# Performance work log

Measured on AMD Instinct MI355X. Metric: run time of the kernel, lower is better.

## Reference

```python
import jax, jax.numpy as jnp
import numpy as np
from jax import lax

DN = ('NHWC', 'HWIO', 'NHWC')

def _conv(x, k, b, stride=1):
    return lax.conv_general_dilated(x, k, (stride, stride), 'SAME', dimension_numbers=DN) + b

def _tconv(x, k, b):
    return lax.conv_transpose(x, k, (2, 2), 'SAME', dimension_numbers=DN) + b


def setup_inputs() -> dict:
    key = jax.random.key(0)
    ks = jax.random.split(key, 32)
    ki = iter(ks)
    def w(shape, scale=0.05):
        return (jax.random.normal(next(ki), shape, dtype=jnp.float32) * scale)
    inp = {}
    inp['x'] = jax.random.uniform(next(ki), (8, 128, 128, 3), dtype=jnp.float32)
    # encoder
    inp['k1'],  inp['b1']  = w((11, 11, 3, 32)),   jnp.zeros((32,), jnp.float32)
    inp['k1c'], inp['b1c'] = w((3, 3, 32, 32)),    jnp.zeros((32,), jnp.float32)
    inp['k2'],  inp['b2']  = w((11, 11, 32, 64)),  jnp.zeros((64,), jnp.float32)
    inp['k2c'], inp['b2c'] = w((3, 3, 64, 64)),    jnp.zeros((64,), jnp.float32)
    inp['k3'],  inp['b3']  = w((11, 11, 64, 128)), jnp.zeros((128,), jnp.float32)
    inp['k3c'], inp['b3c'] = w((3, 3, 128, 128)),  jnp.zeros((128,), jnp.float32)
    # codebook (codebookSize=256, latent dim 128)
    inp['codebook'] = w((256, 128), 0.1)
    # decoder
    inp['tk1'],  inp['tb1']  = w((5, 5, 128, 64)), jnp.zeros((64,), jnp.float32)
    inp['tk1c'], inp['tb1c'] = w((3, 3, 64, 64)),  jnp.zeros((64,), jnp.float32)
    inp['tk2'],  inp['tb2']  = w((5, 5, 64, 32)),  jnp.zeros((32,), jnp.float32)
    inp['tk2c'], inp['tb2c'] = w((3, 3, 32, 32)),  jnp.zeros((32,), jnp.float32)
    inp['tk3'],  inp['tb3']  = w((5, 5, 32, 32)),  jnp.zeros((32,), jnp.float32)
    inp['tk3c'], inp['tb3c'] = w((3, 3, 32, 3)),   jnp.zeros((3,), jnp.float32)
    return inp


def reference(x, k1, b1, k1c, b1c, k2, b2, k2c, b2c, k3, b3, k3c, b3c,
              codebook, tk1, tb1, tk1c, tb1c, tk2, tb2, tk2c, tb2c,
              tk3, tb3, tk3c, tb3c):
    act = jax.nn.silu  # flax.nnx.swish
    # encoder
    d1 = act(_conv(x, k1, b1, 2))
    d1 = act(_conv(d1, k1c, b1c, 1))
    d2 = act(_conv(d1, k2, b2, 2))
    d2 = act(_conv(d2, k2c, b2c, 1))
    d3 = act(_conv(d2, k3, b3, 2))
    d3 = _conv(d3, k3c, b3c, 1)               # [B, H/8, W/8, 128]
    # vector quantization: squared L2 to each codebook entry
    lat = d3.reshape(-1, 1, 128)              # [N, 1, 128]
    eu_dis = jnp.sum((lat - codebook[None]) ** 2, axis=-1)   # [N, 256]
    idx = jnp.argmin(eu_dis, axis=-1)         # [N]
    quantized = jnp.take(codebook, idx, axis=0).reshape(d3.shape)
    # straight-through estimator
    replaced = lax.stop_gradient(quantized - d3) + d3
    # decoder
    d4 = act(_tconv(replaced, tk1, tb1))
    d4 = act(_conv(d4, tk1c, tb1c, 1))
    d5 = act(_tconv(d4, tk2, tb2))
    d5 = act(_conv(d5, tk2c, tb2c, 1))
    d6 = act(_tconv(d5, tk3, tb3))
    out = _conv(d6, tk3c, tb3c, 1)            # [B, H, W, 3]
    return out
```

## Files before the change

### kernel.cpp

```cpp
#include <hip/hip_runtime.h>

#define DI __device__ __forceinline__
DI float silu_f(float x){ return x * (1.0f/(1.0f+__expf(-x))); }

template<int X> struct LOG2 { static constexpr int v = 1 + LOG2<X/2>::v; };
template<> struct LOG2<1> { static constexpr int v = 0; };

template<int KH,int KW,int STRIDE,int PAD,int CIN,int COUT,int NPIX,
         bool ACT,bool BIAS,int G,int CS,int TOW,int FG>
__global__ __launch_bounds__(256) void conv_k(
    const float* __restrict__ in, const float* __restrict__ w,
    const float* __restrict__ bias, float* __restrict__ out,
    const float* __restrict__ fb, size_t fstr,
    int N,int H,int W,int OH,int OW)
{
  constexpr int CLEN = CIN/G;
  constexpr int COB  = COUT/CS;
  constexpr int COQ  = COB/4;
  constexpr int GSH  = LOG2<G>::v;
  constexpr int CSH  = LOG2<CS>::v;
  constexpr int TAPF = CLEN*COB;
  constexpr bool SALL = (KH*KW*TAPF*4) <= 47*1024;
  constexpr int NTAP = SALL ? KH*KW : KW;
  constexpr bool DBUF = (TOW>0) && !SALL && (CLEN!=3) && (FG==0);
  static_assert(CLEN==3 || (CLEN%4)==0, "ci");
  static_assert(FG==0 || (TOW>0 && CLEN!=3), "fg");
  __shared__ float sw[(DBUF?2:1)*NTAP*TAPF];
  constexpr int SPAN = (TOW>0) ? (TOW-1)*STRIDE + KW : 1;
  constexpr int ROWS = (TOW>0) ? ((256/COQ)*NPIX)/TOW : 1;
  constexpr int CQ4  = (TOW>0 && CLEN!=3) ? CLEN/4 : 1;
  constexpr int SI_F = (TOW==0) ? 1 : (CLEN==3 ? ROWS*SPAN*3 : ROWS*CQ4*SPAN*4);
  __shared__ float si[(DBUF?2:1)*SI_F];
  static_assert(TOW==0 || NPIX<=2, "tow npix");
  static_assert(TOW==0 || ((256/COQ)*NPIX) % TOW == 0, "rows");

  const int g  = blockIdx.x & (G-1);
  const int cs = (blockIdx.x >> GSH) & (CS-1);
  const int bx = blockIdx.x >> (GSH+CSH);
  const int total = N*OH*OW;
  if (G>1) out += (size_t)g * total * COUT;
  const int ci_off  = g*CLEN;
  const int co_base = cs*COB;

  int idx = bx*256 + (int)threadIdx.x;
  int cq = idx % COQ;
  int pg = idx / COQ;
  int co = cq*4;
  int gco = co_base + co;
  int p0 = pg*NPIX;

  float acc[NPIX][4] = {};
  int iy0[NPIX], ix0[NPIX]; const float* base[NPIX]; bool pv[NPIX];
#pragma unroll
  for (int t=0;t<NPIX;t++){
    int p=p0+t; pv[t]=(p<total); int pp=pv[t]?p:0;
    int ox=pp%OW; int r=pp/OW; int oy=r%OH; int n=r/OH;
    iy0[t]=oy*STRIDE-PAD; ix0[t]=ox*STRIDE-PAD;
    base[t]=in+(size_t)n*H*W*CIN + ci_off;
  }

  auto stage = [&](int tap0, float* dst){
    constexpr int TQ = TAPF/4;
    constexpr int V  = NTAP*TQ;
    for (int v=threadIdx.x; v<V; v+=256){
      int tap = v / TQ; int rem = v - tap*TQ;
      float4 q;
      if constexpr (CS==1){
        const float4* src = (const float4*)(w + ((size_t)(tap0+tap)*CIN + ci_off)*COUT);
        q = src[rem];
      } else if constexpr (CLEN==3){
        int ci = rem / (COB/4); int r2 = rem - ci*(COB/4);
        q = *(const float4*)(w + ((size_t)(tap0+tap)*CIN + ci)*COUT
                               + co_base + r2*4);
      } else {
        int ci = rem / (COB/4); int r2 = rem - ci*(COB/4);
        q = *(const float4*)(w + ((size_t)(tap0+tap)*CIN + ci_off + ci)*COUT
                               + co_base + r2*4);
      }
      *(float4*)(dst + (size_t)tap*TAPF + rem*4) = q;
    }
  };

  if constexpr (SALL){
    stage(0, sw);
    __syncthreads();
  }

  if constexpr (TOW>0){
    const int pb0 = bx * ((256/COQ)*NPIX);
    const int r0  = pb0 / TOW;
    const int oy0 = r0 % OH;
    const int n0  = r0 / OH;
    int myrow[NPIX], oxl[NPIX];
#pragma unroll
    for (int t=0;t<NPIX;t++){
      int pl = p0 + t - pb0;
      myrow[t] = pl / TOW;
      oxl[t]   = pl - myrow[t]*TOW;
    }

    auto stage_in = [&](int ky, float* dsi){
      if constexpr (CLEN==3){
        constexpr int INS = ROWS*SPAN;
        for (int v=(int)threadIdx.x; v<INS; v+=256){
          int r  = v / SPAN;
          int ixo= v - r*SPAN;
          int iy = (oy0+r)*STRIDE - PAD + ky;
          int ix = ixo - PAD;
          bool ok = iy>=0 && iy<H && ix>=0 && ix<W;
          const float* ip = in + ((size_t)(n0*H+iy)*W + ix)*CIN;
          dsi[v*3+0] = ok?ip[0]:0.f;
          dsi[v*3+1] = ok?ip[1]:0.f;
          dsi[v*3+2] = ok?ip[2]:0.f;
        }
      } else {
        constexpr int INQ = ROWS*CQ4*SPAN;
        for (int v=(int)threadIdx.x; v<INQ; v+=256){
          int r  = v / (CQ4*SPAN);
          int rm = v - r*(CQ4*SPAN);
          int q  = rm / SPAN;
          int ixo= rm - q*SPAN;
          int iy = (oy0+r)*STRIDE - PAD + ky;
          int ix = ixo - PAD;
          bool ok = iy>=0 && iy<H && ix>=0 && ix<W;
          float4 val = make_float4(0.f,0.f,0.f,0.f);
          if (ok){
            size_t off = ((size_t)(n0*H+iy)*W + ix)*CIN + ci_off + q*4;
            if constexpr (FG>0){
              float a[4]; *(float4*)a = *(const float4*)(in + off);
#pragma unroll
              for (int g2=1; g2<FG; g2++){
                float b[4]; *(float4*)b = *(const float4*)(in + (size_t)g2*fstr + off);
#pragma unroll
                for (int j=0;j<4;j++) a[j]+=b[j];
              }
              float bb[4]; *(float4*)bb = *(const float4*)(fb + ci_off + q*4);
#pragma unroll
              for (int j=0;j<4;j++) a[j] = silu_f(a[j]+bb[j]);
              val = *(float4*)a;
            } else {
              val = *(const float4*)(in + off);
            }
          }
          *(float4*)&dsi[(size_t)v*4] = val;
        }
      }
    };

    auto compute_ky = [&](const float* swr, const float* sib){
      for (int kx=0; kx<KW; kx++){
        const float* swt = swr + (size_t)kx*TAPF;
        if constexpr (CLEN==3){
          float wv[3][4];
          *(float4*)wv[0]=*(const float4*)(swt + 0*COB + co);
          *(float4*)wv[1]=*(const float4*)(swt + 1*COB + co);
          *(float4*)wv[2]=*(const float4*)(swt + 2*COB + co);
#pragma unroll
          for (int t=0;t<NPIX;t++){
            const float* sp = &sib[(size_t)(myrow[t]*SPAN + oxl[t]*STRIDE + kx)*3];
            float v0=sp[0], v1=sp[1], v2=sp[2];
#pragma unroll
            for (int j=0;j<4;j++)
              acc[t][j]=fmaf(v0,wv[0][j],fmaf(v1,wv[1][j],fmaf(v2,wv[2][j],acc[t][j])));
          }
        } else {
#pragma unroll 2
          for (int c=0; c<CQ4; c++){
            float wv[4][4];
#pragma unroll
            for (int r=0;r<4;r++)
              *(float4*)wv[r] = *(const float4*)(swt + (c*4+r)*COB + co);
#pragma unroll
            for (int t=0;t<NPIX;t++){
              float va[4];
              *(float4*)va = *(const float4*)&sib[(size_t)((myrow[t]*CQ4 + c)*SPAN + oxl[t]*STRIDE + kx)*4];
#pragma unroll
              for (int r=0;r<4;r++)
#pragma unroll
                for (int j=0;j<4;j++)
                  acc[t][j]=fmaf(va[r],wv[r][j],acc[t][j]);
            }
          }
        }
      }
    };

    if constexpr (DBUF){
      stage(0, sw);
      stage_in(0, si);
      __syncthreads();
      for (int ky=0; ky<KH; ky++){
        const int cur = ky&1, nxt = cur^1;
        if (ky+1<KH){
          stage((ky+1)*KW, sw + (size_t)nxt*NTAP*TAPF);
          stage_in(ky+1, si + (size_t)nxt*SI_F);
        }
        compute_ky(sw + (size_t)cur*NTAP*TAPF, si + (size_t)cur*SI_F);
        __syncthreads();
      }
    } else {
      for (int ky=0; ky<KH; ky++){
        __syncthreads();
        if constexpr (!SALL) stage(ky*KW, sw);
        stage_in(ky, si);
        __syncthreads();
        const float* swr = SALL ? sw + (size_t)ky*KW*TAPF : sw;
        compute_ky(swr, si);
      }
    }
  } else {
    for (int ky=0; ky<KH; ky++){
      if constexpr (!SALL){
        __syncthreads();
        stage(ky*KW, sw);
        __syncthreads();
      }
      const float* swr = SALL ? sw + (size_t)ky*KW*TAPF : sw;
      for (int kx=0; kx<KW; kx++){
        const float* swt = swr + (size_t)kx*TAPF;
        const float* ip[NPIX]; bool ok[NPIX];
#pragma unroll
        for (int t=0;t<NPIX;t++){
          int iy=iy0[t]+ky, ix=ix0[t]+kx;
          ok[t]=pv[t] && iy>=0 && iy<H && ix>=0 && ix<W;
          ip[t]=base[t]+(size_t)(iy*W+ix)*CIN;
        }
        if constexpr (CLEN==3){
          float wv[3][4];
          *(float4*)wv[0]=*(const float4*)(swt + 0*COB + co);
          *(float4*)wv[1]=*(const float4*)(swt + 1*COB + co);
          *(float4*)wv[2]=*(const float4*)(swt + 2*COB + co);
#pragma unroll
          for (int t=0;t<NPIX;t++){
            float v0=ok[t]?ip[t][0]:0.f;
            float v1=ok[t]?ip[t][1]:0.f;
            float v2=ok[t]?ip[t][2]:0.f;
#pragma unroll
            for (int j=0;j<4;j++)
              acc[t][j]=fmaf(v0,wv[0][j],fmaf(v1,wv[1][j],fmaf(v2,wv[2][j],acc[t][j])));
          }
        } else {
#pragma unroll 2
          for (int ci=0; ci<CLEN; ci+=4){
            float wv[4][4];
#pragma unroll
            for (int r=0;r<4;r++)
              *(float4*)wv[r] = *(const float4*)(swt + (ci+r)*COB + co);
#pragma unroll
            for (int t=0;t<NPIX;t++){
              float va[4];
              *(float4*)va = ok[t] ? *(const float4*)(ip[t]+ci)
                                   : make_float4(0.f,0.f,0.f,0.f);
#pragma unroll
              for (int r=0;r<4;r++)
#pragma unroll
                for (int j=0;j<4;j++)
                  acc[t][j]=fmaf(va[r],wv[r][j],acc[t][j]);
            }
          }
        }
      }
    }
  }

  float bv[4]={0.f,0.f,0.f,0.f};
  if constexpr (BIAS) *(float4*)bv = *(const float4*)(bias+gco);
#pragma unroll
  for (int t=0;t<NPIX;t++) if (pv[t]){
    float o[4];
#pragma unroll
    for (int j=0;j<4;j++){
      float v = acc[t][j]+bv[j];
      o[j] = ACT ? silu_f(v) : v;
    }
    *(float4*)(out + (size_t)(p0+t)*COUT + gco) = *(float4*)o;
  }
}

template<int CIN,int COUT,int NPIX,int G,int CS,int IW,bool DIRECT,int FG>
__global__ __launch_bounds__(256) void tconv_rb(
    const float* __restrict__ in, const float* __restrict__ w,
    const float* __restrict__ bias, float* __restrict__ out,
    const float* __restrict__ fb, size_t fstr,
    int N,int H,int W,int OH,int OW)
{
  constexpr int CLEN = CIN/G;
  constexpr int COB  = COUT/CS;
  constexpr int COQ  = COB/4;
  constexpr int GSH  = LOG2<G>::v;
  constexpr int CSH  = LOG2<CS>::v;
  constexpr int TAPF = CLEN*COB;
  constexpr int PPB  = (256/COQ)*NPIX;
  static_assert(PPB % IW == 0, "whole rows");
  constexpr int ROWS_O = PPB/IW;
  constexpr int NRI  = ROWS_O + 2;
  constexpr int SPAN = IW + 2;
  constexpr int CQ4  = CLEN/4;
  __shared__ float sw[9*TAPF];
  __shared__ float si[NRI*CQ4*SPAN*4];

  const int par = blockIdx.x & 3;
  const int py = par>>1, px = par&1;
  const int g  = (blockIdx.x>>2) & (G-1);
  const int cs = (blockIdx.x>>(2+GSH)) & (CS-1);
  const int bx = blockIdx.x >> (2+GSH+CSH);
  const int NKY = py?3:2, NKX = px?3:2;
  const int OHh = OH>>1;
  if (G>1) out += (size_t)g * (size_t)N*OH*OW*COUT;
  const int co_base = cs*COB;

  const int tid = (int)threadIdx.x;
  int idx = bx*256 + tid;
  int cq = idx % COQ;
  int pg = idx / COQ;
  int co = cq*4;
  int p0 = pg*NPIX;
  const int pb0 = bx*PPB;
  const int R0  = pb0 / IW;
  const int oy0 = R0 % OHh;
  const int n0  = R0 / OHh;

  int myrow[NPIX], xx[NPIX];
#pragma unroll
  for (int t=0;t<NPIX;t++){
    int lp = p0 + t - pb0;
    myrow[t] = lp / IW;
    xx[t]    = lp - myrow[t]*IW;
  }

  {
    constexpr int TQ = TAPF/4;
    const int V = NKY*NKX*TQ;
    for (int v=tid; v<V; v+=256){
      int tap = v / TQ; int rem = v - tap*TQ;
      int j = tap / NKX, i = tap - j*NKX;
      int ky = 2*j + (py?0:1), kx = 2*i + (px?0:1);
      int ci = rem / (COB/4); int r2 = rem - ci*(COB/4);
      float4 q = *(const float4*)(w + ((size_t)(ky*5+kx)*CIN + g*CLEN + ci)*COUT
                                    + co_base + r2*4);
      *(float4*)(sw + (size_t)(j*3+i)*TAPF + rem*4) = q;
    }
  }
  {
    constexpr int INQ = NRI*CQ4*SPAN;
    for (int v=tid; v<INQ; v+=256){
      int r  = v / (CQ4*SPAN);
      int rm = v - r*(CQ4*SPAN);
      int q  = rm / SPAN;
      int cc = rm - q*SPAN;
      int iy = oy0 - 1 + r;
      int ix = cc - 1;
      bool ok = iy>=0 && iy<H && ix>=0 && ix<W;
      float4 val = make_float4(0.f,0.f,0.f,0.f);
      if (ok){
        size_t off = ((size_t)(n0*H+iy)*W + ix)*CIN + g*CLEN + q*4;
        if constexpr (FG>0){
          float a[4]; *(float4*)a = *(const float4*)(in + off);
#pragma unroll
          for (int g2=1; g2<FG; g2++){
            float b[4]; *(float4*)b = *(const float4*)(in + (size_t)g2*fstr + off);
#pragma unroll
            for (int j=0;j<4;j++) a[j]+=b[j];
          }
          float bb[4]; *(float4*)bb = *(const float4*)(fb + g*CLEN + q*4);
#pragma unroll
          for (int j=0;j<4;j++) a[j] = silu_f(a[j]+bb[j]);
          val = *(float4*)a;
        } else {
          val = *(const float4*)(in + off);
        }
      }
      *(float4*)&si[(size_t)v*4] = val;
    }
  }
  __syncthreads();

  float acc[NPIX][4] = {};
  for (int j=0;j<NKY;j++){
    for (int i=0;i<NKX;i++){
      const float* swt = sw + (size_t)(j*3+i)*TAPF;
#pragma unroll 2
      for (int c=0;c<CQ4;c++){
        float wv[4][4];
#pragma unroll
        for (int r=0;r<4;r++)
          *(float4*)wv[r] = *(const float4*)(swt + (c*4+r)*COB + co);
#pragma unroll
        for (int t=0;t<NPIX;t++){
          float va[4];
          *(float4*)va = *(const float4*)&si[(size_t)(((myrow[t]+j)*CQ4 + c)*SPAN + (xx[t]+i))*4];
#pragma unroll
          for (int r=0;r<4;r++)
#pragma unroll
            for (int jj=0;jj<4;jj++)
              acc[t][jj]=fmaf(va[r],wv[r][jj],acc[t][jj]);
        }
      }
    }
  }

  float bv[4]={0.f,0.f,0.f,0.f};
  if constexpr (DIRECT) *(float4*)bv = *(const float4*)(bias+co_base+co);
#pragma unroll
  for (int t=0;t<NPIX;t++){
    float o[4];
#pragma unroll
    for (int jj=0;jj<4;jj++){
      float v = acc[t][jj]+bv[jj];
      o[jj] = DIRECT ? silu_f(v) : v;
    }
    *(float4*)(out + (((size_t)n0*OH + (2*(oy0+myrow[t])+py))*OW + (2*xx[t]+px))*COUT + co_base+co) = *(float4*)o;
  }
}

__global__ __launch_bounds__(256) void vq_k(
    const float* __restrict__ p, const float* __restrict__ bias,
    const float* __restrict__ cb, float* __restrict__ q, int NLat)
{
  __shared__ float slat[4][128];
  int wave = threadIdx.x >> 6;
  int lane = threadIdx.x & 63;
  int l = blockIdx.x*4 + wave;
  if (l >= NLat) return;
  const float* p0 = p + (size_t)l*128;
  const float* p1 = p0 + (size_t)NLat*128;
  slat[wave][lane]    = p0[lane]    + p1[lane]    + bias[lane];
  slat[wave][lane+64] = p0[lane+64] + p1[lane+64] + bias[lane+64];

  float bestd = INFINITY; int besti = 0;
  for (int c0=0;c0<256;c0+=64){
    int c = c0 + lane;
    const float* cp = cb + (size_t)c*128;
    float d = 0.f;
#pragma unroll 8
    for (int k=0;k<128;k+=4){
      float4 cv = *reinterpret_cast<const float4*>(cp+k);
      float d0 = slat[wave][k+0]-cv.x;
      float d1 = slat[wave][k+1]-cv.y;
      float d2 = slat[wave][k+2]-cv.z;
      float d3 = slat[wave][k+3]-cv.w;
      d += d0*d0; d += d1*d1; d += d2*d2; d += d3*d3;
    }
    if (d < bestd) { bestd = d; besti = c; }
  }
  for (int off=32; off; off>>=1){
    float od = __shfl_down(bestd, off);
    int   oi = __shfl_down(besti, off);
    if (od < bestd || (od == bestd && oi < besti)) { bestd=od; besti=oi; }
  }
  besti = __shfl(besti, 0);
  const float* cp = cb + (size_t)besti*128;
  float* qp = q + (size_t)l*128;
  qp[lane]    = cp[lane];
  qp[lane+64] = cp[lane+64];
}

__global__ __launch_bounds__(256) void conv_last_k(
    const float* __restrict__ in, const float* __restrict__ w,
    float* __restrict__ p, int N,int H,int W)
{
  int g = blockIdx.x % 3;
  int bx = blockIdx.x / 3;
  int pix = bx*256 + threadIdx.x;
  int total = N*H*W;
  if (pix>=total) return;
  int x = pix % W; int r = pix / W; int y = r % H; int n = r / H;
  float a0=0.f, a1=0.f, a2=0.f;
  int iy = y + g - 1;
  if (iy>=0 && iy<H){
    const float* base = in + ((size_t)n*H + iy)*W*32;
    for (int kx=0;kx<3;kx++){
      int ix=x+kx-1; if(ix<0||ix>=W) continue;
      const float* ip = base + (size_t)ix*32;
      const float* wp = w + (size_t)((g*3+kx)*32)*3;
#pragma unroll
      for (int ci=0;ci<32;ci+=4){
        float va[4]; *(float4*)va = *(const float4*)(ip+ci);
        float wv[12];
        *(float4*)(wv+0) = *(const float4*)(wp+ci*3+0);
        *(float4*)(wv+4) = *(const float4*)(wp+ci*3+4);
        *(float4*)(wv+8) = *(const float4*)(wp+ci*3+8);
#pragma unroll
        for (int r2=0;r2<4;r2++){
          a0 = fmaf(va[r2], wv[r2*3+0], a0);
          a1 = fmaf(va[r2], wv[r2*3+1], a1);
          a2 = fmaf(va[r2], wv[r2*3+2], a2);
        }
      }
    }
  }
  float* pp = p + (size_t)g*total*3 + (size_t)pix*3;
  pp[0]=a0; pp[1]=a1; pp[2]=a2;
}

__global__ __launch_bounds__(256) void reduce_last_k(
    const float* __restrict__ p, const float* __restrict__ bias,
    float* __restrict__ out, int n)
{
  int i = (blockIdx.x*256+threadIdx.x)*4;
  if (i>=n) return;
  float a[4]; *(float4*)a = *(const float4*)(p+i);
#pragma unroll
  for (int g=1; g<3; g++){
    float b[4]; *(float4*)b = *(const float4*)(p+(size_t)g*n+i);
#pragma unroll
    for (int j=0;j<4;j++) a[j]+=b[j];
  }
  float o[4];
#pragma unroll
  for (int j=0;j<4;j++) o[j] = a[j] + bias[(i+j)%3];
  *(float4*)(out+i) = *(float4*)o;
}

extern "C" void kernel_launch(void* const* d_in, const int* in_sizes, int n_in,
                              void* d_out, int out_size, void* d_ws, size_t ws_size,
                              hipStream_t stream) {
  const float* x    = (const float*)d_in[0];
  const float* k1   = (const float*)d_in[1];  const float* b1  = (const float*)d_in[2];
  const float* k1c  = (const float*)d_in[3];  const float* b1c = (const float*)d_in[4];
  const float* k2   = (const float*)d_in[5];  const float* b2  = (const float*)d_in[6];
  const float* k2c  = (const float*)d_in[7];  const float* b2c = (const float*)d_in[8];
  const float* k3   = (const float*)d_in[9];  const float* b3  = (const float*)d_in[10];
  const float* k3c  = (const float*)d_in[11]; const float* b3c = (const float*)d_in[12];
  const float* cb   = (const float*)d_in[13];
  const float* tk1  = (const float*)d_in[14]; const float* tb1  = (const float*)d_in[15];
  const float* tk1c = (const float*)d_in[16]; const float* tb1c = (const float*)d_in[17];
  const float* tk2  = (const float*)d_in[18]; const float* tb2  = (const float*)d_in[19];
  const float* tk2c = (const float*)d_in[20]; const float* tb2c = (const float*)d_in[21];
  const float* tk3  = (const float*)d_in[22]; const float* tb3  = (const float*)d_in[23];
  const float* tk3c = (const float*)d_in[24]; const float* tb3c = (const float*)d_in[25];
  float* out = (float*)d_out;

  float* S  = (float*)d_ws;
  float* W0 = S;
  float* W1 = S + 1048576;
  float* PA = S + 2097152;
  float* PB = S + 3145728;
  float* PC = S + 2097152;
  float* PD = S + 2097152;
  float* PE = S + 4194304;
  float* PF = S + 2097152;
  float* PG = S + 2097152;
  dim3 blk(256);

  conv_k<11,11,2,4,  3, 32,2,true ,true ,1,2,64,0><<< 512,blk,0,stream>>>(x,  k1,  b1,  W0, nullptr,0, 8,128,128,64,64);
  conv_k< 3, 3,1,1, 32, 32,2,true ,true ,1,2,64,0><<< 512,blk,0,stream>>>(W0, k1c, b1c, W1, nullptr,0, 8,64,64,64,64);
  conv_k<11,11,2,4, 32, 64,2,false,false,2,2,32,0><<< 512,blk,0,stream>>>(W1, k2,  nullptr, PA, nullptr,0, 8,64,64,32,32);
  conv_k< 3, 3,1,1, 64, 64,1,true ,true ,1,2,32,2><<< 512,blk,0,stream>>>(PA, k2c, b2c, W0, b2,524288, 8,32,32,32,32);
  conv_k<11,11,2,4, 64,128,2,false,false,4,4,16,0><<< 512,blk,0,stream>>>(W0, k3,  nullptr, PB, nullptr,0, 8,32,32,16,16);
  conv_k< 3, 3,1,1,128,128,1,false,false,2,4,16,4><<< 512,blk,0,stream>>>(PB, k3c, nullptr, PC, b3,262144, 8,16,16,16,16);
  vq_k<<<512,blk,0,stream>>>(PC, b3c, cb, W1, 2048);
  tconv_rb<128,64,1,4,2,16,false,0><<<2048,blk,0,stream>>>(W1, tk1, nullptr, PD, nullptr,0, 8,16,16,32,32);
  conv_k< 3, 3,1,1, 64, 64,2,false,false,2,4,32,4><<< 512,blk,0,stream>>>(PD, tk1c, nullptr, PE, tb1,524288, 8,32,32,32,32);
  tconv_rb< 64,32,1,2,1,32,false,2><<<2048,blk,0,stream>>>(PE, tk2, nullptr, PF, tb1c,524288, 8,32,32,64,64);
  conv_k< 3, 3,1,1, 32, 32,2,true ,true ,1,2,64,2><<< 512,blk,0,stream>>>(PF, tk2c, tb2c, W1, tb2,1048576, 8,64,64,64,64);
  tconv_rb< 32,32,1,1,2,64,true ,0><<<4096,blk,0,stream>>>(W1, tk3, tb3, PG, nullptr,0, 8,64,64,128,128);
  conv_last_k<<<1536,blk,0,stream>>>(PG, tk3c, S, 8,128,128);
  reduce_last_k<<<384,blk,0,stream>>>(S, tb3c, out, 393216);
}
```

Before: 451.0 us.

## Pad 3-channel input tiles to float4 and fuse final conv with reduction

The first conv's 3-channel shared-memory input tile is padded to 4 floats per pixel so that staging and compute use single float4 accesses instead of scalar loads. The last 3x3 conv no longer splits the kernel rows across three blocks with a separate reduction kernel. Each thread now runs all nine taps, adds the bias and writes the output directly. This removes one launch and a partial-sum round trip through global memory, at the cost of fewer blocks (less parallelism) and slightly more shared memory in the first conv.

Measured after the change: 447.0 us. About the same (-0.9%).

```diff
diff --git a/kernel.cpp b/kernel.cpp
--- a/kernel.cpp
+++ b/kernel.cpp
@@ -29,7 +29,7 @@
   constexpr int SPAN = (TOW>0) ? (TOW-1)*STRIDE + KW : 1;
   constexpr int ROWS = (TOW>0) ? ((256/COQ)*NPIX)/TOW : 1;
   constexpr int CQ4  = (TOW>0 && CLEN!=3) ? CLEN/4 : 1;
-  constexpr int SI_F = (TOW==0) ? 1 : (CLEN==3 ? ROWS*SPAN*3 : ROWS*CQ4*SPAN*4);
+  constexpr int SI_F = (TOW==0) ? 1 : (CLEN==3 ? ROWS*SPAN*4 : ROWS*CQ4*SPAN*4);
   __shared__ float si[(DBUF?2:1)*SI_F];
   static_assert(TOW==0 || NPIX<=2, "tow npix");
   static_assert(TOW==0 || ((256/COQ)*NPIX) % TOW == 0, "rows");
@@ -109,9 +109,8 @@
           int ix = ixo - PAD;
           bool ok = iy>=0 && iy<H && ix>=0 && ix<W;
           const float* ip = in + ((size_t)(n0*H+iy)*W + ix)*CIN;
-          dsi[v*3+0] = ok?ip[0]:0.f;
-          dsi[v*3+1] = ok?ip[1]:0.f;
-          dsi[v*3+2] = ok?ip[2]:0.f;
+          float v0 = ok?ip[0]:0.f, v1 = ok?ip[1]:0.f, v2 = ok?ip[2]:0.f;
+          *(float4*)&dsi[(size_t)v*4] = make_float4(v0,v1,v2,0.f);
         }
       } else {
         constexpr int INQ = ROWS*CQ4*SPAN;
@@ -157,11 +156,11 @@
           *(float4*)wv[2]=*(const float4*)(swt + 2*COB + co);
 #pragma unroll
           for (int t=0;t<NPIX;t++){
-            const float* sp = &sib[(size_t)(myrow[t]*SPAN + oxl[t]*STRIDE + kx)*3];
-            float v0=sp[0], v1=sp[1], v2=sp[2];
+            float vq4[4];
+            *(float4*)vq4 = *(const float4*)&sib[(size_t)(myrow[t]*SPAN + oxl[t]*STRIDE + kx)*4];
 #pragma unroll
             for (int j=0;j<4;j++)
-              acc[t][j]=fmaf(v0,wv[0][j],fmaf(v1,wv[1][j],fmaf(v2,wv[2][j],acc[t][j])));
+              acc[t][j]=fmaf(vq4[0],wv[0][j],fmaf(vq4[1],wv[1][j],fmaf(vq4[2],wv[2][j],acc[t][j])));
           }
         } else {
 #pragma unroll 2
@@ -457,22 +456,19 @@
 
 __global__ __launch_bounds__(256) void conv_last_k(
     const float* __restrict__ in, const float* __restrict__ w,
-    float* __restrict__ p, int N,int H,int W)
+    const float* __restrict__ bias, float* __restrict__ out,
+    int N,int H,int W)
 {
-  int g = blockIdx.x % 3;
-  int bx = blockIdx.x / 3;
-  int pix = bx*256 + threadIdx.x;
+  int p = blockIdx.x*256 + threadIdx.x;
   int total = N*H*W;
-  if (pix>=total) return;
-  int x = pix % W; int r = pix / W; int y = r % H; int n = r / H;
-  float a0=0.f, a1=0.f, a2=0.f;
-  int iy = y + g - 1;
-  if (iy>=0 && iy<H){
-    const float* base = in + ((size_t)n*H + iy)*W*32;
-    for (int kx=0;kx<3;kx++){
-      int ix=x+kx-1; if(ix<0||ix>=W) continue;
-      const float* ip = base + (size_t)ix*32;
-      const float* wp = w + (size_t)((g*3+kx)*32)*3;
+  if (p>=total) return;
+  int x = p % W; int r = p / W; int y = r % H; int n = r / H;
+  float a0=bias[0], a1=bias[1], a2=bias[2];
+  const float* base = in + (size_t)n*H*W*32;
+  for (int ky=0;ky<3;ky++){ int iy=y+ky-1; if(iy<0||iy>=H) continue;
+    for (int kx=0;kx<3;kx++){ int ix=x+kx-1; if(ix<0||ix>=W) continue;
+      const float* ip = base + (size_t)(iy*W+ix)*32;
+      const float* wp = w + (size_t)((ky*3+kx)*32)*3;
 #pragma unroll
       for (int ci=0;ci<32;ci+=4){
         float va[4]; *(float4*)va = *(const float4*)(ip+ci);
@@ -489,27 +485,7 @@
       }
     }
   }
-  float* pp = p + (size_t)g*total*3 + (size_t)pix*3;
-  pp[0]=a0; pp[1]=a1; pp[2]=a2;
-}
-
-__global__ __launch_bounds__(256) void reduce_last_k(
-    const float* __restrict__ p, const float* __restrict__ bias,
-    float* __restrict__ out, int n)
-{
-  int i = (blockIdx.x*256+threadIdx.x)*4;
-  if (i>=n) return;
-  float a[4]; *(float4*)a = *(const float4*)(p+i);
-#pragma unroll
-  for (int g=1; g<3; g++){
-    float b[4]; *(float4*)b = *(const float4*)(p+(size_t)g*n+i);
-#pragma unroll
-    for (int j=0;j<4;j++) a[j]+=b[j];
-  }
-  float o[4];
-#pragma unroll
-  for (int j=0;j<4;j++) o[j] = a[j] + bias[(i+j)%3];
-  *(float4*)(out+i) = *(float4*)o;
+  out[(size_t)p*3+0]=a0; out[(size_t)p*3+1]=a1; out[(size_t)p*3+2]=a2;
 }
 
 extern "C" void kernel_launch(void* const* d_in, const int* in_sizes, int n_in,
@@ -555,6 +531,5 @@
   tconv_rb< 64,32,1,2,1,32,false,2><<<2048,blk,0,stream>>>(PE, tk2, nullptr, PF, tb1c,524288, 8,32,32,64,64);
   conv_k< 3, 3,1,1, 32, 32,2,true ,true ,1,2,64,2><<< 512,blk,0,stream>>>(PF, tk2c, tb2c, W1, tb2,1048576, 8,64,64,64,64);
   tconv_rb< 32,32,1,1,2,64,true ,0><<<4096,blk,0,stream>>>(W1, tk3, tb3, PG, nullptr,0, 8,64,64,128,128);
-  conv_last_k<<<1536,blk,0,stream>>>(PG, tk3c, S, 8,128,128);
-  reduce_last_k<<<384,blk,0,stream>>>(S, tb3c, out, 393216);
+  conv_last_k<<<512,blk,0,stream>>>(PG, tk3c, tb3c, out, 8,128,128);
 }
```
